# Performance work log

Hardware: AMD Instinct MI355X
Metric: run time of the kernel (lower is better)

## Reference

```python
import jax, jax.numpy as jnp
import numpy as np
from jax import lax

CHUNK = 512  # query-point chunk for pairwise point-triangle distance
EPS = 1e-12
LOSS_WEIGHT = 1.0


def closest_point_on_tri(p, a, b, c):
    """Closest point on triangle (a,b,c) to p. Broadcasts over leading dims; last dim = 3.
    Ericson, Real-Time Collision Detection, ch. 5.1.5."""
    ab = b - a
    ac = c - a
    ap = p - a
    d1 = (ab * ap).sum(-1)
    d2 = (ac * ap).sum(-1)
    bp = p - b
    d3 = (ab * bp).sum(-1)
    d4 = (ac * bp).sum(-1)
    cp_ = p - c
    d5 = (ab * cp_).sum(-1)
    d6 = (ac * cp_).sum(-1)
    va = d3 * d6 - d5 * d4
    vb = d5 * d2 - d1 * d6
    vc = d1 * d4 - d3 * d2
    # edge / interior parameters (denominators guarded; masks pick valid regions)
    v_ab = (d1 / jnp.maximum(d1 - d3, EPS))[..., None]
    w_ac = (d2 / jnp.maximum(d2 - d6, EPS))[..., None]
    w_bc = ((d4 - d3) / jnp.maximum((d4 - d3) + (d5 - d6), EPS))[..., None]
    denom = jnp.maximum(va + vb + vc, EPS)
    v_in = (vb / denom)[..., None]
    w_in = (vc / denom)[..., None]
    cond1 = ((d1 <= 0) & (d2 <= 0))[..., None]            # vertex a
    cond2 = ((d3 >= 0) & (d4 <= d3))[..., None]           # vertex b
    cond3 = ((d6 >= 0) & (d5 <= d6))[..., None]           # vertex c
    cond4 = ((vc <= 0) & (d1 >= 0) & (d3 <= 0))[..., None]  # edge ab
    cond5 = ((vb <= 0) & (d2 >= 0) & (d6 <= 0))[..., None]  # edge ac
    cond6 = ((va <= 0) & ((d4 - d3) >= 0) & ((d5 - d6) >= 0))[..., None]  # edge bc
    out = a + ab * v_in + ac * w_in                      # interior
    out = jnp.where(cond6, b + (c - b) * w_bc, out)
    out = jnp.where(cond5, a + ac * w_ac, out)
    out = jnp.where(cond4, a + ab * v_ab, out)
    out = jnp.where(cond3, c, out)
    out = jnp.where(cond2, b, out)
    out = jnp.where(cond1, a, out)
    return out


def nearest_points_on_mesh(points, verts, faces):
    """Exact nearest point on mesh surface for each query point.
    points: [P,3], verts: [V,3], faces: [F,3] int. Returns cp [P,3]."""
    ta = verts[faces[:, 0]]  # [F,3]
    tb = verts[faces[:, 1]]
    tc = verts[faces[:, 2]]

    def chunk_argmin(pc):  # pc: [CHUNK,3]
        cp = closest_point_on_tri(pc[:, None, :], ta[None], tb[None], tc[None])  # [C,F,3]
        d2 = ((pc[:, None, :] - cp) ** 2).sum(-1)  # [C,F]
        return jnp.argmin(d2, axis=1)

    P = points.shape[0]
    idx = lax.map(chunk_argmin, points.reshape(-1, CHUNK, 3)).reshape(P)
    cp = closest_point_on_tri(points, ta[idx], tb[idx], tc[idx])  # [P,3]
    return cp


def _per_batch_loss(points, verts, faces):
    cp = nearest_points_on_mesh(points, verts, faces)
    # torch.norm(resid, p=2) is the Frobenius norm of the whole [P,3] residual (scalar);
    # closest point is detached in the original autograd.Function usage.
    resid = points - lax.stop_gradient(cp)
    dist = jnp.sqrt((resid ** 2).sum())
    height = verts[:, 1].max() - verts[:, 1].min()  # bbox_3d[1]
    return dist / height


def setup_inputs() -> dict:
    key = jax.random.key(0)
    k1, k2, k3 = jax.random.split(key, 3)
    B, P, V, F = 2, 8192, 4098, 8192
    body_verts = jax.random.normal(k1, (B, P, 3), dtype=jnp.float32)
    mesh_verts = jax.random.normal(k2, (B, V, 3), dtype=jnp.float32)
    faces = jax.random.randint(k3, (B, F, 3), 0, V, dtype=jnp.int32)
    return {"body_verts": body_verts, "mesh_verts": mesh_verts, "faces": faces}


def reference(body_verts, mesh_verts, faces):
    losses = jax.vmap(_per_batch_loss)(body_verts, mesh_verts, faces)  # [B]
    return jnp.mean(losses) * LOSS_WEIGHT
```

## Files before the change

### kernel.cpp

```cpp
#include <hip/hip_runtime.h>

#define EPSF 1e-12f
constexpr int BB = 2;
constexpr int PP = 8192;
constexpr int VV = 4098;
constexpr int FF = 8192;

constexpr int FAST_F4 = 6;
constexpr int SLOW_F4 = 5;
constexpr int PTS_PER_BLOCK = 2048;
constexpr int NSLICES = 256;
constexpr int CHUNK_T = FF / NSLICES;

typedef float f2 __attribute__((ext_vector_type(2)));

__device__ __forceinline__ f2 vfma(f2 a, f2 b, f2 c) {
#if __has_builtin(__builtin_elementwise_fma)
    return __builtin_elementwise_fma(a, b, c);
#else
    return (f2){fmaf(a.x, b.x, c.x), fmaf(a.y, b.y, c.y)};
#endif
}
__device__ __forceinline__ f2 vmin2(f2 a, f2 b) { return __builtin_elementwise_min(a, b); }
__device__ __forceinline__ f2 vmax2(f2 a, f2 b) { return __builtin_elementwise_max(a, b); }
__device__ __forceinline__ f2 bc(float s) { return (f2){s, s}; }

__global__ __launch_bounds__(256) void precompute_kernel(
    const float* __restrict__ verts, const int* __restrict__ faces,
    float4* __restrict__ fastrec, float4* __restrict__ slowrec,
    unsigned long long* __restrict__ mask, unsigned int* __restrict__ minD,
    float* __restrict__ out)
{
    int idx = blockIdx.x * 256 + threadIdx.x;
    if (idx == 0) out[0] = 0.0f;
    if (idx < BB * PP) minD[idx] = 0x7F800000u;
    if (idx >= BB * FF) return;

    int b = idx / FF;
    const float* vb = verts + (size_t)b * VV * 3;
    int i0 = faces[idx * 3 + 0];
    int i1 = faces[idx * 3 + 1];
    int i2 = faces[idx * 3 + 2];

    float ax = vb[i0*3+0], ay = vb[i0*3+1], az = vb[i0*3+2];
    float bx = vb[i1*3+0], by = vb[i1*3+1], bz = vb[i1*3+2];
    float cx = vb[i2*3+0], cy = vb[i2*3+1], cz = vb[i2*3+2];

    float abx = bx-ax, aby = by-ay, abz = bz-az;
    float acx = cx-ax, acy = cy-ay, acz = cz-az;
    float bcx = cx-bx, bcy = cy-by, bcz = cz-bz;

    {
        float4* t = slowrec + (size_t)idx * SLOW_F4;
        t[0] = make_float4(ax, ay, az, abx);
        t[1] = make_float4(bx, by, bz, aby);
        t[2] = make_float4(cx, cy, cz, abz);
        t[3] = make_float4(acx, acy, acz, bcx);
        t[4] = make_float4(bcy, bcz, 0.0f, 0.0f);
    }

    float nx = aby*acz - abz*acy;
    float ny = abz*acx - abx*acz;
    float nz = abx*acy - aby*acx;

    float ka1  = abx*ax + aby*ay + abz*az;
    float ka2  = acx*ax + acy*ay + acz*az;
    float kan  = nx*ax + ny*ay + nz*az;
    float aa   = ax*ax + ay*ay + az*az;
    float abac = abx*acx + aby*acy + abz*acz;

    float ab2 = abx*abx + aby*aby + abz*abz;
    float ac2 = acx*acx + acy*acy + acz*acz;
    float bc2 = bcx*bcx + bcy*bcy + bcz*bcz;
    float nn  = nx*nx + ny*ny + nz*nz;

    float inv_ab2 = 1.0f / fmaxf(ab2, EPSF);
    float inv_ac2 = 1.0f / fmaxf(ac2, EPSF);
    float inv_bc2 = 1.0f / fmaxf(bc2, EPSF);
    float inv_nn  = 1.0f / fmaxf(nn,  EPSF);

    bool slowtri = !((nn > 0.03f * (ab2 * ac2)) &&
                     (ab2 > 1e-4f) && (ac2 > 1e-4f) && (bc2 > 1e-4f));

    unsigned long long mb = __ballot(slowtri);
    if ((threadIdx.x & 63) == 0) mask[idx >> 6] = mb;

    float INF = __uint_as_float(0x7F800000u);
    float4* f = fastrec + (size_t)idx * FAST_F4;
    f[0] = make_float4(abx, aby, abz, ka1);
    f[1] = make_float4(acx, acy, acz, ka2);
    f[2] = make_float4(nx,  ny,  nz,  slowtri ? INF : kan);
    f[3] = make_float4(ax,  ay,  az,  slowtri ? INF : aa);
    f[4] = make_float4(ab2, ac2, abac, bc2);
    f[5] = make_float4(inv_ab2, inv_ac2, inv_bc2, inv_nn);
}

__device__ __forceinline__ float tri_d2(
    float px, float py, float pz,
    float4 R0, float4 R1, float4 R2, float4 R3, float4 R4)
{
#pragma clang fp contract(off)
    float ax = R0.x, ay = R0.y, az = R0.z;
    float bx = R1.x, by = R1.y, bz = R1.z;
    float cx = R2.x, cy = R2.y, cz = R2.z;
    float abx = R0.w, aby = R1.w, abz = R2.w;
    float acx = R3.x, acy = R3.y, acz = R3.z;
    float bcx = R3.w, bcy = R4.x, bcz = R4.y;

    float apx = px - ax, apy = py - ay, apz = pz - az;
    float d1 = (abx*apx + aby*apy) + abz*apz;
    float d2 = (acx*apx + acy*apy) + acz*apz;
    float bpx = px - bx, bpy = py - by, bpz = pz - bz;
    float d3 = (abx*bpx + aby*bpy) + abz*bpz;
    float d4 = (acx*bpx + acy*bpy) + acz*bpz;
    float cqx = px - cx, cqy = py - cy, cqz = pz - cz;
    float d5 = (abx*cqx + aby*cqy) + abz*cqz;
    float d6 = (acx*cqx + acy*cqy) + acz*cqz;

    float va = d3*d6 - d5*d4;
    float vb = d5*d2 - d1*d6;
    float vc = d1*d4 - d3*d2;
    float u43 = d4 - d3;
    float u56 = d5 - d6;

    bool c1 = (d1 <= 0.0f) && (d2 <= 0.0f);
    bool c2 = (d3 >= 0.0f) && (d4 <= d3);
    bool c3 = (d6 >= 0.0f) && (d5 <= d6);
    bool c4 = (vc <= 0.0f) && (d1 >= 0.0f) && (d3 <= 0.0f);
    bool c5 = (vb <= 0.0f) && (d2 >= 0.0f) && (d6 <= 0.0f);
    bool c6 = (va <= 0.0f) && (u43 >= 0.0f) && (u56 >= 0.0f);

    int reg = c1 ? 0 : (c2 ? 1 : (c3 ? 2 : (c4 ? 3 : (c5 ? 4 : (c6 ? 5 : 6)))));

    float denom = fmaxf((va + vb) + vc, EPSF);
    float den1 = (reg == 3) ? fmaxf(d1 - d3, EPSF)
               : (reg == 5) ? fmaxf(u43 + u56, EPSF)
               : (reg == 6) ? denom : 1.0f;
    float num1 = (reg == 3) ? d1
               : (reg == 5) ? u43
               : (reg == 6) ? vb : 0.0f;
    float den2 = (reg == 4) ? fmaxf(d2 - d6, EPSF)
               : (reg == 6) ? denom : 1.0f;
    float num2 = (reg == 4) ? d2
               : (reg == 6) ? vc : 0.0f;
    float s = num1 / den1;
    float t = num2 / den2;

    bool useB = (reg == 1) || (reg == 5);
    bool useC = (reg == 2);
    float basex = useB ? bx : (useC ? cx : ax);
    float basey = useB ? by : (useC ? cy : ay);
    float basez = useB ? bz : (useC ? cz : az);
    bool e1bc = (reg == 5);
    float e1x = e1bc ? bcx : abx;
    float e1y = e1bc ? bcy : aby;
    float e1z = e1bc ? bcz : abz;

    float cpx = (basex + e1x*s) + acx*t;
    float cpy = (basey + e1y*s) + acy*t;
    float cpz = (basez + e1z*s) + acz*t;
    float rx = px - cpx, ry = py - cpy, rz = pz - cpz;
    return (rx*rx + ry*ry) + rz*rz;
}

__device__ __forceinline__ f2 fast_d2_pk(
    f2 px, f2 py, f2 pz, f2 pp,
    float4 F0, float4 F1, float4 F2, float4 F3, float4 F4, float4 F5)
{
    const float INF = __uint_as_float(0x7F800000u);

    f2 sab = vfma(bc(F0.x), px, vfma(bc(F0.y), py, bc(F0.z) * pz));
    f2 sac = vfma(bc(F1.x), px, vfma(bc(F1.y), py, bc(F1.z) * pz));
    f2 sn  = vfma(bc(F2.x), px, vfma(bc(F2.y), py, bc(F2.z) * pz));
    f2 adp = vfma(bc(F3.x), px, vfma(bc(F3.y), py, bc(F3.z) * pz));

    f2 d1 = sab - bc(F0.w), d2 = sac - bc(F1.w);
    f2 d3 = d1 - bc(F4.x);
    f2 d4 = d2 - bc(F4.z);
    f2 d5 = d1 - bc(F4.z);
    f2 d6 = d2 - bc(F4.y);
    f2 tp = sn - bc(F2.w);

    f2 ap2 = vfma(bc(-2.0f), adp, pp) + bc(F3.w);
    f2 bp2 = vfma(bc(-2.0f), d1, ap2) + bc(F4.x);

    f2 sA = vmin2(vmax2(d1 * bc(F5.x), bc(0.0f)), bc(1.0f));
    f2 dAB = vfma(-sA, vfma(-sA, bc(F4.x), d1 + d1), ap2);
    f2 sC = vmin2(vmax2(d2 * bc(F5.y), bc(0.0f)), bc(1.0f));
    f2 dAC = vfma(-sC, vfma(-sC, bc(F4.y), d2 + d2), ap2);
    f2 u43 = d4 - d3;
    f2 sB = vmin2(vmax2(u43 * bc(F5.z), bc(0.0f)), bc(1.0f));
    f2 dBC = vfma(-sB, vfma(-sB, bc(F4.w), u43 + u43), bp2);

    f2 va = vfma(d3, d6, -(d5 * d4));
    f2 vb = vfma(d5, d2, -(d1 * d6));
    f2 vc = vfma(d1, d4, -(d3 * d2));
    f2 mv = vmin2(vmin2(va, vb), vc);
    f2 dIN = (tp * tp) * bc(F5.w);

    f2 dI;
    dI.x = (mv.x >= 0.0f) ? dIN.x : INF;
    dI.y = (mv.y >= 0.0f) ? dIN.y : INF;

    return vmin2(vmin2(dAB, dAC), vmin2(dBC, dI));
}

__global__ __launch_bounds__(256) void dist_kernel(
    const float* __restrict__ pts, const float4* __restrict__ fa,
    const float4* __restrict__ sa, const unsigned long long* __restrict__ mask,
    unsigned int* __restrict__ minD)
{
    int tid   = threadIdx.x;
    int pg    = blockIdx.x;
    int slice = blockIdx.y;

    int b  = pg / (PP / PTS_PER_BLOCK);
    int p0 = pg * PTS_PER_BLOCK + tid;

    f2 px[4], py[4], pz[4], pp[4], m[4];
    int pidx[8];
#pragma unroll
    for (int k = 0; k < 4; ++k) {
        int pa = p0 + (2*k)   * 256;
        int pb = p0 + (2*k+1) * 256;
        pidx[2*k] = pa; pidx[2*k+1] = pb;
        px[k] = (f2){pts[pa*3+0], pts[pb*3+0]};
        py[k] = (f2){pts[pa*3+1], pts[pb*3+1]};
        pz[k] = (f2){pts[pa*3+2], pts[pb*3+2]};
        pp[k] = vfma(px[k], px[k], vfma(py[k], py[k], pz[k] * pz[k]));
        m[k] = bc(__uint_as_float(0x7F800000u));
    }

    int t0 = b * FF + slice * CHUNK_T;
    const float4* fb = fa + (size_t)t0 * FAST_F4;

    for (int t = 0; t < CHUNK_T; ++t) {
        float4 F0 = fb[t*FAST_F4+0];
        float4 F1 = fb[t*FAST_F4+1];
        float4 F2 = fb[t*FAST_F4+2];
        float4 F3 = fb[t*FAST_F4+3];
        float4 F4 = fb[t*FAST_F4+4];
        float4 F5 = fb[t*FAST_F4+5];
#pragma unroll
        for (int k = 0; k < 4; ++k)
            m[k] = vmin2(m[k], fast_d2_pk(px[k], py[k], pz[k], pp[k],
                                          F0, F1, F2, F3, F4, F5));
    }

    unsigned long long bits =
        (mask[t0 >> 6] >> (t0 & 63)) & 0xFFFFFFFFull;
    while (bits) {
        int bit = __builtin_ctzll(bits);
        bits &= bits - 1;
        const float4* sb = sa + (size_t)(t0 + bit) * SLOW_F4;
        float4 S0 = sb[0], S1 = sb[1], S2 = sb[2], S3 = sb[3], S4 = sb[4];
#pragma unroll
        for (int k = 0; k < 4; ++k) {
            m[k].x = fminf(m[k].x, tri_d2(px[k].x, py[k].x, pz[k].x, S0, S1, S2, S3, S4));
            m[k].y = fminf(m[k].y, tri_d2(px[k].y, py[k].y, pz[k].y, S0, S1, S2, S3, S4));
        }
    }

#pragma unroll
    for (int k = 0; k < 4; ++k) {
        atomicMin(&minD[pidx[2*k]],   __float_as_uint(fmaxf(m[k].x, 0.0f)));
        atomicMin(&minD[pidx[2*k+1]], __float_as_uint(fmaxf(m[k].y, 0.0f)));
    }
}

__global__ __launch_bounds__(256) void reduce_kernel(
    const unsigned int* __restrict__ minD, const float* __restrict__ verts,
    float* __restrict__ out)
{
    int b = blockIdx.x;
    int tid = threadIdx.x;

    float s = 0.0f;
    for (int i = tid; i < PP; i += 256)
        s += __uint_as_float(minD[b * PP + i]);

    float ymin = 3.4e38f, ymax = -3.4e38f;
    for (int i = tid; i < VV; i += 256) {
        float y = verts[((size_t)b * VV + i) * 3 + 1];
        ymin = fminf(ymin, y); ymax = fmaxf(ymax, y);
    }

    for (int off = 32; off > 0; off >>= 1) {
        s += __shfl_down(s, off);
        ymin = fminf(ymin, __shfl_down(ymin, off));
        ymax = fmaxf(ymax, __shfl_down(ymax, off));
    }

    __shared__ float shs[4], shmn[4], shmx[4];
    if ((tid & 63) == 0) {
        int w = tid >> 6;
        shs[w] = s; shmn[w] = ymin; shmx[w] = ymax;
    }
    __syncthreads();
    if (tid == 0) {
        float tot = shs[0], mn = shmn[0], mx = shmx[0];
        for (int w = 1; w < 4; ++w) {
            tot += shs[w];
            mn = fminf(mn, shmn[w]);
            mx = fmaxf(mx, shmx[w]);
        }
        atomicAdd(out, 0.5f * sqrtf(tot) / (mx - mn));
    }
}

extern "C" void kernel_launch(void* const* d_in, const int* in_sizes, int n_in,
                              void* d_out, int out_size, void* d_ws, size_t ws_size,
                              hipStream_t stream) {
    const float* pts   = (const float*)d_in[0];
    const float* verts = (const float*)d_in[1];
    const int*   faces = (const int*)d_in[2];
    float* out = (float*)d_out;

    char* w = (char*)d_ws;
    float4* fastrec = (float4*)w;
    w += (size_t)BB * FF * FAST_F4 * sizeof(float4);
    float4* slowrec = (float4*)w;
    w += (size_t)BB * FF * SLOW_F4 * sizeof(float4);
    unsigned long long* mask = (unsigned long long*)w;
    w += (size_t)(BB * FF / 64) * sizeof(unsigned long long);
    unsigned int* minD = (unsigned int*)w;

    precompute_kernel<<<(BB * FF + 255) / 256, 256, 0, stream>>>(
        verts, faces, fastrec, slowrec, mask, minD, out);

    dim3 grid(BB * PP / PTS_PER_BLOCK, NSLICES);
    dist_kernel<<<grid, 256, 0, stream>>>(pts, fastrec, slowrec, mask, minD);

    reduce_kernel<<<BB, 256, 0, stream>>>(minD, verts, out);
}
```

Baseline: 217.0 us.

## Pack triangle pairs into interleaved layout and vectorize across triangles

The precompute kernel now writes triangle constants interleaved for pairs of triangles, so the distance kernel's packed-float2 math runs over two triangles per query point instead of two points per triangle. Each thread now handles 4 points, with points per block halved to 1024 so the grid doubles. Constant loads become float2 per field, which may be less efficient than float4 loads. The final reduction is split across 16 blocks using order-preserving float keys for min/max, plus a tiny finalize kernel.

```diff
diff --git a/kernel.cpp b/kernel.cpp
--- a/kernel.cpp
+++ b/kernel.cpp
@@ -6,9 +6,9 @@
 constexpr int VV = 4098;
 constexpr int FF = 8192;
 
-constexpr int FAST_F4 = 6;
 constexpr int SLOW_F4 = 5;
-constexpr int PTS_PER_BLOCK = 2048;
+constexpr int NCONST = 24;
+constexpr int PTS_PER_BLOCK = 1024;
 constexpr int NSLICES = 256;
 constexpr int CHUNK_T = FF / NSLICES;
 
@@ -25,14 +25,24 @@
 __device__ __forceinline__ f2 vmax2(f2 a, f2 b) { return __builtin_elementwise_max(a, b); }
 __device__ __forceinline__ f2 bc(float s) { return (f2){s, s}; }
 
+__device__ __forceinline__ unsigned int fkey(float f) {
+    unsigned int u = __float_as_uint(f);
+    return (u >> 31) ? ~u : (u | 0x80000000u);
+}
+__device__ __forceinline__ float funkey(unsigned int k) {
+    unsigned int u = (k >> 31) ? (k ^ 0x80000000u) : ~k;
+    return __uint_as_float(u);
+}
+
 __global__ __launch_bounds__(256) void precompute_kernel(
     const float* __restrict__ verts, const int* __restrict__ faces,
-    float4* __restrict__ fastrec, float4* __restrict__ slowrec,
+    float* __restrict__ pairrec, float4* __restrict__ slowrec,
     unsigned long long* __restrict__ mask, unsigned int* __restrict__ minD,
-    float* __restrict__ out)
+    float* __restrict__ sums, unsigned int* __restrict__ ykmin,
+    unsigned int* __restrict__ ykmax)
 {
     int idx = blockIdx.x * 256 + threadIdx.x;
-    if (idx == 0) out[0] = 0.0f;
+    if (idx < BB) { sums[idx] = 0.0f; ykmin[idx] = 0xFFFFFFFFu; ykmax[idx] = 0u; }
     if (idx < BB * PP) minD[idx] = 0x7F800000u;
     if (idx >= BB * FF) return;
 
@@ -86,13 +96,17 @@
     if ((threadIdx.x & 63) == 0) mask[idx >> 6] = mb;
 
     float INF = __uint_as_float(0x7F800000u);
-    float4* f = fastrec + (size_t)idx * FAST_F4;
-    f[0] = make_float4(abx, aby, abz, ka1);
-    f[1] = make_float4(acx, acy, acz, ka2);
-    f[2] = make_float4(nx,  ny,  nz,  slowtri ? INF : kan);
-    f[3] = make_float4(ax,  ay,  az,  slowtri ? INF : aa);
-    f[4] = make_float4(ab2, ac2, abac, bc2);
-    f[5] = make_float4(inv_ab2, inv_ac2, inv_bc2, inv_nn);
+    float cvals[NCONST] = {
+        abx, aby, abz, ka1,
+        acx, acy, acz, ka2,
+        nx,  ny,  nz,  slowtri ? INF : kan,
+        ax,  ay,  az,  slowtri ? INF : aa,
+        ab2, ac2, abac, bc2,
+        inv_ab2, inv_ac2, inv_bc2, inv_nn
+    };
+    float* pr = pairrec + (size_t)(idx >> 1) * (2 * NCONST) + (idx & 1);
+#pragma unroll
+    for (int c = 0; c < NCONST; ++c) pr[2*c] = cvals[c];
 }
 
 __device__ __forceinline__ float tri_d2(
@@ -163,53 +177,12 @@
     return (rx*rx + ry*ry) + rz*rz;
 }
 
-__device__ __forceinline__ f2 fast_d2_pk(
-    f2 px, f2 py, f2 pz, f2 pp,
-    float4 F0, float4 F1, float4 F2, float4 F3, float4 F4, float4 F5)
-{
-    const float INF = __uint_as_float(0x7F800000u);
-
-    f2 sab = vfma(bc(F0.x), px, vfma(bc(F0.y), py, bc(F0.z) * pz));
-    f2 sac = vfma(bc(F1.x), px, vfma(bc(F1.y), py, bc(F1.z) * pz));
-    f2 sn  = vfma(bc(F2.x), px, vfma(bc(F2.y), py, bc(F2.z) * pz));
-    f2 adp = vfma(bc(F3.x), px, vfma(bc(F3.y), py, bc(F3.z) * pz));
-
-    f2 d1 = sab - bc(F0.w), d2 = sac - bc(F1.w);
-    f2 d3 = d1 - bc(F4.x);
-    f2 d4 = d2 - bc(F4.z);
-    f2 d5 = d1 - bc(F4.z);
-    f2 d6 = d2 - bc(F4.y);
-    f2 tp = sn - bc(F2.w);
-
-    f2 ap2 = vfma(bc(-2.0f), adp, pp) + bc(F3.w);
-    f2 bp2 = vfma(bc(-2.0f), d1, ap2) + bc(F4.x);
-
-    f2 sA = vmin2(vmax2(d1 * bc(F5.x), bc(0.0f)), bc(1.0f));
-    f2 dAB = vfma(-sA, vfma(-sA, bc(F4.x), d1 + d1), ap2);
-    f2 sC = vmin2(vmax2(d2 * bc(F5.y), bc(0.0f)), bc(1.0f));
-    f2 dAC = vfma(-sC, vfma(-sC, bc(F4.y), d2 + d2), ap2);
-    f2 u43 = d4 - d3;
-    f2 sB = vmin2(vmax2(u43 * bc(F5.z), bc(0.0f)), bc(1.0f));
-    f2 dBC = vfma(-sB, vfma(-sB, bc(F4.w), u43 + u43), bp2);
-
-    f2 va = vfma(d3, d6, -(d5 * d4));
-    f2 vb = vfma(d5, d2, -(d1 * d6));
-    f2 vc = vfma(d1, d4, -(d3 * d2));
-    f2 mv = vmin2(vmin2(va, vb), vc);
-    f2 dIN = (tp * tp) * bc(F5.w);
-
-    f2 dI;
-    dI.x = (mv.x >= 0.0f) ? dIN.x : INF;
-    dI.y = (mv.y >= 0.0f) ? dIN.y : INF;
-
-    return vmin2(vmin2(dAB, dAC), vmin2(dBC, dI));
-}
-
 __global__ __launch_bounds__(256) void dist_kernel(
-    const float* __restrict__ pts, const float4* __restrict__ fa,
+    const float* __restrict__ pts, const f2* __restrict__ pair,
     const float4* __restrict__ sa, const unsigned long long* __restrict__ mask,
     unsigned int* __restrict__ minD)
 {
+    const float INF = __uint_as_float(0x7F800000u);
     int tid   = threadIdx.x;
     int pg    = blockIdx.x;
     int slice = blockIdx.y;
@@ -217,34 +190,64 @@
     int b  = pg / (PP / PTS_PER_BLOCK);
     int p0 = pg * PTS_PER_BLOCK + tid;
 
-    f2 px[4], py[4], pz[4], pp[4], m[4];
-    int pidx[8];
+    float PX[4], PY[4], PZ[4];
+    f2 X[4], Y[4], Z[4], W[4], m[4];
 #pragma unroll
     for (int k = 0; k < 4; ++k) {
-        int pa = p0 + (2*k)   * 256;
-        int pb = p0 + (2*k+1) * 256;
-        pidx[2*k] = pa; pidx[2*k+1] = pb;
-        px[k] = (f2){pts[pa*3+0], pts[pb*3+0]};
-        py[k] = (f2){pts[pa*3+1], pts[pb*3+1]};
-        pz[k] = (f2){pts[pa*3+2], pts[pb*3+2]};
-        pp[k] = vfma(px[k], px[k], vfma(py[k], py[k], pz[k] * pz[k]));
-        m[k] = bc(__uint_as_float(0x7F800000u));
+        int p = p0 + k * 256;
+        PX[k] = pts[p*3+0]; PY[k] = pts[p*3+1]; PZ[k] = pts[p*3+2];
+        X[k] = bc(PX[k]); Y[k] = bc(PY[k]); Z[k] = bc(PZ[k]);
+        W[k] = vfma(X[k], X[k], vfma(Y[k], Y[k], Z[k] * Z[k]));
+        m[k] = bc(INF);
     }
 
     int t0 = b * FF + slice * CHUNK_T;
-    const float4* fb = fa + (size_t)t0 * FAST_F4;
-
-    for (int t = 0; t < CHUNK_T; ++t) {
-        float4 F0 = fb[t*FAST_F4+0];
-        float4 F1 = fb[t*FAST_F4+1];
-        float4 F2 = fb[t*FAST_F4+2];
-        float4 F3 = fb[t*FAST_F4+3];
-        float4 F4 = fb[t*FAST_F4+4];
-        float4 F5 = fb[t*FAST_F4+5];
-#pragma unroll
-        for (int k = 0; k < 4; ++k)
-            m[k] = vmin2(m[k], fast_d2_pk(px[k], py[k], pz[k], pp[k],
-                                          F0, F1, F2, F3, F4, F5));
+    const f2* cb = pair + (size_t)(t0 >> 1) * NCONST;
+
+    for (int tp = 0; tp < CHUNK_T / 2; ++tp) {
+        const f2* c = cb + tp * NCONST;
+        f2 abx=c[0], aby=c[1], abz=c[2], ka1=c[3];
+        f2 acx=c[4], acy=c[5], acz=c[6], ka2=c[7];
+        f2 nx=c[8],  ny=c[9],  nz=c[10], kan=c[11];
+        f2 ax=c[12], ay=c[13], az=c[14], aa=c[15];
+        f2 ab2=c[16], ac2=c[17], abac=c[18], bc2=c[19];
+        f2 iab2=c[20], iac2=c[21], ibc2=c[22], inn=c[23];
+
+#pragma unroll
+        for (int k = 0; k < 4; ++k) {
+            f2 sab = vfma(abx, X[k], vfma(aby, Y[k], abz * Z[k]));
+            f2 sac = vfma(acx, X[k], vfma(acy, Y[k], acz * Z[k]));
+            f2 sn  = vfma(nx,  X[k], vfma(ny,  Y[k], nz  * Z[k]));
+            f2 adp = vfma(ax,  X[k], vfma(ay,  Y[k], az  * Z[k]));
+
+            f2 d1 = sab - ka1, d2 = sac - ka2;
+            f2 d3 = d1 - ab2, d4 = d2 - abac;
+            f2 d5 = d1 - abac, d6 = d2 - ac2;
+            f2 tpn = sn - kan;
+
+            f2 ap2 = vfma(bc(-2.0f), adp, W[k]) + aa;
+            f2 bp2 = vfma(bc(-2.0f), d1, ap2) + ab2;
+
+            f2 sA = vmin2(vmax2(d1 * iab2, bc(0.0f)), bc(1.0f));
+            f2 dAB = vfma(-sA, vfma(-sA, ab2, d1 + d1), ap2);
+            f2 sC = vmin2(vmax2(d2 * iac2, bc(0.0f)), bc(1.0f));
+            f2 dAC = vfma(-sC, vfma(-sC, ac2, d2 + d2), ap2);
+            f2 u43 = d4 - d3;
+            f2 sB = vmin2(vmax2(u43 * ibc2, bc(0.0f)), bc(1.0f));
+            f2 dBC = vfma(-sB, vfma(-sB, bc2, u43 + u43), bp2);
+
+            f2 va = vfma(d3, d6, -(d5 * d4));
+            f2 vb = vfma(d5, d2, -(d1 * d6));
+            f2 vc = vfma(d1, d4, -(d3 * d2));
+            f2 mv = vmin2(vmin2(va, vb), vc);
+            f2 dIN = (tpn * tpn) * inn;
+
+            f2 dI;
+            dI.x = (mv.x >= 0.0f) ? dIN.x : INF;
+            dI.y = (mv.y >= 0.0f) ? dIN.y : INF;
+
+            m[k] = vmin2(m[k], vmin2(vmin2(dAB, dAC), vmin2(dBC, dI)));
+        }
     }
 
     unsigned long long bits =
@@ -255,32 +258,34 @@
         const float4* sb = sa + (size_t)(t0 + bit) * SLOW_F4;
         float4 S0 = sb[0], S1 = sb[1], S2 = sb[2], S3 = sb[3], S4 = sb[4];
 #pragma unroll
-        for (int k = 0; k < 4; ++k) {
-            m[k].x = fminf(m[k].x, tri_d2(px[k].x, py[k].x, pz[k].x, S0, S1, S2, S3, S4));
-            m[k].y = fminf(m[k].y, tri_d2(px[k].y, py[k].y, pz[k].y, S0, S1, S2, S3, S4));
-        }
+        for (int k = 0; k < 4; ++k)
+            m[k].x = fminf(m[k].x, tri_d2(PX[k], PY[k], PZ[k], S0, S1, S2, S3, S4));
     }
 
 #pragma unroll
     for (int k = 0; k < 4; ++k) {
-        atomicMin(&minD[pidx[2*k]],   __float_as_uint(fmaxf(m[k].x, 0.0f)));
-        atomicMin(&minD[pidx[2*k+1]], __float_as_uint(fmaxf(m[k].y, 0.0f)));
-    }
-}
-
-__global__ __launch_bounds__(256) void reduce_kernel(
+        float r = fminf(m[k].x, m[k].y);
+        atomicMin(&minD[p0 + k*256], __float_as_uint(fmaxf(r, 0.0f)));
+    }
+}
+
+__global__ __launch_bounds__(256) void reduce1_kernel(
     const unsigned int* __restrict__ minD, const float* __restrict__ verts,
-    float* __restrict__ out)
-{
-    int b = blockIdx.x;
+    float* __restrict__ sums, unsigned int* __restrict__ ykmin,
+    unsigned int* __restrict__ ykmax)
+{
+    int blk = blockIdx.x;
+    int b = blk >> 3, part = blk & 7;
     int tid = threadIdx.x;
 
     float s = 0.0f;
-    for (int i = tid; i < PP; i += 256)
+    int i0 = part * (PP / 8), i1 = i0 + (PP / 8);
+    for (int i = i0 + tid; i < i1; i += 256)
         s += __uint_as_float(minD[b * PP + i]);
 
     float ymin = 3.4e38f, ymax = -3.4e38f;
-    for (int i = tid; i < VV; i += 256) {
+    int v0 = part * 513, v1 = min(v0 + 513, VV);
+    for (int i = v0 + tid; i < v1; i += 256) {
         float y = verts[((size_t)b * VV + i) * 3 + 1];
         ymin = fminf(ymin, y); ymax = fmaxf(ymax, y);
     }
@@ -304,7 +309,23 @@
             mn = fminf(mn, shmn[w]);
             mx = fmaxf(mx, shmx[w]);
         }
-        atomicAdd(out, 0.5f * sqrtf(tot) / (mx - mn));
+        atomicAdd(&sums[b], tot);
+        atomicMin(&ykmin[b], fkey(mn));
+        atomicMax(&ykmax[b], fkey(mx));
+    }
+}
+
+__global__ __launch_bounds__(64) void reduce2_kernel(
+    const float* __restrict__ sums, const unsigned int* __restrict__ ykmin,
+    const unsigned int* __restrict__ ykmax, float* __restrict__ out)
+{
+    if (threadIdx.x == 0) {
+        float r = 0.0f;
+        for (int b = 0; b < BB; ++b) {
+            float h = funkey(ykmax[b]) - funkey(ykmin[b]);
+            r += sqrtf(sums[b]) / h;
+        }
+        out[0] = r * 0.5f;
     }
 }
 
@@ -317,19 +338,24 @@
     float* out = (float*)d_out;
 
     char* w = (char*)d_ws;
-    float4* fastrec = (float4*)w;
-    w += (size_t)BB * FF * FAST_F4 * sizeof(float4);
+    float* pairrec = (float*)w;
+    w += (size_t)(BB * FF / 2) * (2 * NCONST) * sizeof(float);
     float4* slowrec = (float4*)w;
     w += (size_t)BB * FF * SLOW_F4 * sizeof(float4);
     unsigned long long* mask = (unsigned long long*)w;
     w += (size_t)(BB * FF / 64) * sizeof(unsigned long long);
     unsigned int* minD = (unsigned int*)w;
+    w += (size_t)BB * PP * sizeof(unsigned int);
+    float* sums = (float*)w;          w += BB * sizeof(float);
+    unsigned int* ykmin = (unsigned int*)w; w += BB * sizeof(unsigned int);
+    unsigned int* ykmax = (unsigned int*)w;
 
     precompute_kernel<<<(BB * FF + 255) / 256, 256, 0, stream>>>(
-        verts, faces, fastrec, slowrec, mask, minD, out);
+        verts, faces, pairrec, slowrec, mask, minD, sums, ykmin, ykmax);
 
     dim3 grid(BB * PP / PTS_PER_BLOCK, NSLICES);
-    dist_kernel<<<grid, 256, 0, stream>>>(pts, fastrec, slowrec, mask, minD);
-
-    reduce_kernel<<<BB, 256, 0, stream>>>(minD, verts, out);
-}
+    dist_kernel<<<grid, 256, 0, stream>>>(pts, (const f2*)pairrec, slowrec, mask, minD);
+
+    reduce1_kernel<<<16, 256, 0, stream>>>(minD, verts, sums, ykmin, ykmax);
+    reduce2_kernel<<<1, 64, 0, stream>>>(sums, ykmin, ykmax, out);
+}
```

Measured after the change: 208.8 us. -3.8%, faster.
